# Kernel optimization log

Measured on AMD Instinct MI355X. Metric: run time of the kernel, lower is better.

## Reference

```python
import jax, jax.numpy as jnp
import numpy as np

K = 5  # filter_size
EPS = 1e-5

def conv1x1(x, w):
    # x: [B,Ci,H,W], w: [Co,Ci]
    return jnp.einsum('bihw,oi->bohw', x, w)

def layernorm_c(x, g, b):
    # LayerNorm over channel dim of NCHW (torch permutes to NHWC, norms last dim)
    m = x.mean(axis=1, keepdims=True)
    v = x.var(axis=1, keepdims=True)
    xn = (x - m) / jnp.sqrt(v + EPS)
    return xn * g[None, :, None, None] + b[None, :, None, None]

def conv3x3(x, w):
    return jax.lax.conv_general_dilated(x, w, (1, 1), [(1, 1), (1, 1)],
                                        dimension_numbers=('NCHW', 'OIHW', 'NCHW'))

def apply_dyn_filter(feat, filt):
    # feat: [B,C,H,W]; filt: [B,C*K*K,H,W] ordered as C x (K*K row-major), matching
    # torch .view(B,C,K*K,H,W) and F.unfold channel layout.
    B, C, H, W = feat.shape
    f = filt.reshape(B, C, K * K, H, W)
    p = K // 2
    fp = jnp.pad(feat, ((0, 0), (0, 0), (p, p), (p, p)))  # zero pad, same as F.unfold
    out = jnp.zeros_like(feat)
    for ki in range(K):
        for kj in range(K):
            out = out + fp[:, :, ki:ki + H, kj:kj + W] * f[:, :, ki * K + kj]
    return out


def setup_inputs() -> dict:
    key = jax.random.key(0)
    ks = jax.random.split(key, 9)
    B, Cin, H, W = 1, 64, 128, 128
    Ch = 128
    s = lambda fan: 1.0 / np.sqrt(fan)
    inp = {
        'rgb_high': jax.random.normal(ks[0], (B, Cin, H, W), jnp.float32),
        'event':    jax.random.normal(ks[1], (B, Cin, H, W), jnp.float32),
        'conv_w':   jax.random.normal(ks[2], (Ch, Cin), jnp.float32) * s(Cin),
        'ln_g':     jnp.ones((Ch,), jnp.float32),
        'ln_b':     jnp.zeros((Ch,), jnp.float32),
        'df1_w':    jax.random.normal(ks[3], (Ch, Ch, 3, 3), jnp.float32) * s(Ch * 9),
        'df2_w':    jax.random.normal(ks[4], (Ch * K * K, Ch), jnp.float32) * s(Ch),
        'sp_w':     jax.random.normal(ks[5], (Ch, Ch), jnp.float32) * s(Ch),
        'out_w':    jax.random.normal(ks[6], (Cin, Ch), jnp.float32) * s(Ch),
    }
    return inp


def reference(rgb_high, event, conv_w, ln_g, ln_b, df1_w, df2_w, sp_w, out_w):
    rgb_feat = layernorm_c(conv1x1(rgb_high, conv_w), ln_g, ln_b)
    ev_feat = layernorm_c(conv1x1(event, conv_w), ln_g, ln_b)
    # dynamic filter generator: conv3x3 -> ReLU -> conv1x1 (shared weights)
    rgb_filter = conv1x1(jax.nn.relu(conv3x3(rgb_feat, df1_w)), df2_w)
    ev_filter = conv1x1(jax.nn.relu(conv3x3(ev_feat, df1_w)), df2_w)
    rgb_en = apply_dyn_filter(rgb_feat, rgb_filter)
    ev_en = apply_dyn_filter(ev_feat, ev_filter)
    rgb_filtered = rgb_en * jax.nn.sigmoid(conv1x1(ev_en, sp_w))
    rgb_fused = rgb_en + rgb_filtered + rgb_feat
    rgb_norm = layernorm_c(rgb_fused, ln_g, ln_b)
    return conv1x1(rgb_norm, out_w)
```

## Files before the change

kernel.cpp:

```cpp
#include <hip/hip_runtime.h>
#include <math.h>

#define HW 16384
#define WD 128
#define HD 128
#define CIN 64
#define CH 128
#define EPSV 1e-5f

typedef __attribute__((ext_vector_type(8))) short short8;
typedef __attribute__((ext_vector_type(4))) short short4v;
typedef __attribute__((ext_vector_type(4))) float f32x4;

__device__ __forceinline__ short f2bf(float x) {
  unsigned u = __float_as_uint(x);
  u += 0x7FFFu + ((u >> 16) & 1u);
  return (short)(u >> 16);
}
__device__ __forceinline__ float bf2f(short x) {
  return __uint_as_float(((unsigned)(unsigned short)x) << 16);
}

__global__ __launch_bounds__(256) void k_prep_misc(
    const float* __restrict__ cw, const float* __restrict__ w3,
    const float* __restrict__ spw, const float* __restrict__ outw,
    const float* __restrict__ rgb, const float* __restrict__ ev,
    short* __restrict__ cwp, short* __restrict__ w3p,
    short* __restrict__ spwp, short* __restrict__ outwp,
    short* __restrict__ xT_rgb, short* __restrict__ xT_ev) {
  int idx = blockIdx.x * 256 + threadIdx.x;
  if (idx < 8192) {
    int j = idx & 7, grp = (idx >> 3) & 3, m = (idx >> 5) & 127, q = idx >> 12;
    cwp[idx] = f2bf(cw[m * CIN + q * 32 + grp * 8 + j]);
  } else if (idx < 155648) {
    int i = idx - 8192;
    int j = i & 7, grp = (i >> 3) & 3, m = (i >> 5) & 127, ks = i >> 12;
    int tap = ks >> 2, q = ks & 3;
    int c = q * 32 + grp * 8 + j;
    w3p[i] = f2bf(w3[(m * CH + c) * 9 + tap]);
  } else if (idx < 172032) {
    int i = idx - 155648;
    int j = i & 7, grp = (i >> 3) & 3, m = (i >> 5) & 127, q = i >> 12;
    spwp[i] = f2bf(spw[m * CH + q * 32 + grp * 8 + j]);
  } else if (idx < 180224) {
    int i = idx - 172032;
    int j = i & 7, grp = (i >> 3) & 3, m = (i >> 5) & 63, q = i >> 11;
    outwp[i] = f2bf(outw[m * CH + q * 32 + grp * 8 + j]);
  } else {
    int i = idx - 180224;
    int img = i >> 14, p = i & 16383;
    const float* x = img ? ev : rgb;
    short* xT = img ? xT_ev : xT_rgb;
#pragma unroll
    for (int cb = 0; cb < 8; ++cb) {
      short8 v;
#pragma unroll
      for (int j = 0; j < 8; ++j) v[j] = f2bf(x[(cb * 8 + j) * HW + p]);
      *(short8*)(xT + p * CIN + cb * 8) = v;
    }
  }
}

__global__ __launch_bounds__(256) void k_prep_df2(const float* __restrict__ df2,
                                                  short* __restrict__ df2p) {
  int idx = blockIdx.x * 256 + threadIdx.x;
  int j = idx & 7;
  int slotp = (idx >> 3) & 511;
  int c = idx >> 12;
  int ms = slotp >> 4, k8l = slotp & 15;
  int k8 = k8l ^ (ms & 7);
  int k = k8 * 8 + j;
  int t;
  if (ms < 16) {
    t = (ms >> 2) * 5 + (ms & 3);
  } else {
    int g = (ms >> 2) & 3, r = ms & 3;
    if (g == 0) t = 20 + r;
    else if (g == 1) t = r * 5 + 4;
    else if (g == 2 && r == 0) t = 24;
    else t = -1;
  }
  float v = (t >= 0) ? df2[(c * 25 + t) * CH + k] : 0.f;
  df2p[idx] = f2bf(v);
}

__global__ __launch_bounds__(256) void k_feat_mfma(
    const short* __restrict__ xT_rgb, const short* __restrict__ xT_ev,
    const short* __restrict__ cwp, const float* __restrict__ g,
    const float* __restrict__ b,
    short* __restrict__ featT_rgb, short* __restrict__ featT_ev) {
  __shared__ float sg[CH], sb[CH];
  int tid = threadIdx.x;
  if (tid < CH) { sg[tid] = g[tid]; sb[tid] = b[tid]; }
  __syncthreads();
  const short* xT = blockIdx.z ? xT_ev : xT_rgb;
  short* featT = blockIdx.z ? featT_ev : featT_rgb;
  int wave = tid >> 6, lane = tid & 63, col = lane & 15, grp = lane >> 4;
  int p = blockIdx.x * 64 + wave * 16 + col;

  const short8* bp = (const short8*)(xT + p * CIN);
  short8 bq0 = bp[grp], bq1 = bp[4 + grp];
  const short8* ap = (const short8*)cwp;

  f32x4 acc[8];
#pragma unroll
  for (int mt = 0; mt < 8; ++mt) {
    acc[mt] = (f32x4){0.f, 0.f, 0.f, 0.f};
    short8 a0 = ap[(0 * 128 + mt * 16 + col) * 4 + grp];
    short8 a1 = ap[(1 * 128 + mt * 16 + col) * 4 + grp];
    acc[mt] = __builtin_amdgcn_mfma_f32_16x16x32_bf16(a0, bq0, acc[mt], 0, 0, 0);
    acc[mt] = __builtin_amdgcn_mfma_f32_16x16x32_bf16(a1, bq1, acc[mt], 0, 0, 0);
  }
  float s = 0.f, s2 = 0.f;
#pragma unroll
  for (int mt = 0; mt < 8; ++mt)
#pragma unroll
    for (int r = 0; r < 4; ++r) { float v = acc[mt][r]; s += v; s2 += v * v; }
  s += __shfl_xor(s, 16);  s += __shfl_xor(s, 32);
  s2 += __shfl_xor(s2, 16); s2 += __shfl_xor(s2, 32);
  float mean = s * (1.f / CH);
  float var = s2 * (1.f / CH) - mean * mean;
  float rinv = rsqrtf(var + EPSV);
#pragma unroll
  for (int mt = 0; mt < 8; ++mt) {
    short4v fv;
#pragma unroll
    for (int r = 0; r < 4; ++r) {
      int m = mt * 16 + grp * 4 + r;
      fv[r] = f2bf((acc[mt][r] - mean) * rinv * sg[m] + sb[m]);
    }
    *(short4v*)(featT + p * CH + mt * 16 + grp * 4) = fv;
  }
}

__global__ __launch_bounds__(256) void k_conv3_v4(
    const short* __restrict__ featT_rgb, const short* __restrict__ featT_ev,
    const short* __restrict__ w3p,
    short* __restrict__ rT_rgb, short* __restrict__ rT_ev) {
  __shared__ short sF[108 * 128];
  const short* featT = blockIdx.z ? featT_ev : featT_rgb;
  short* rT = blockIdx.z ? rT_ev : rT_rgb;
  int tid = threadIdx.x, wave = tid >> 6, lane = tid & 63;
  int col = lane & 15, grp = lane >> 4;
  int ty0 = (blockIdx.x >> 3) * 4;
  int tx0 = (blockIdx.x & 7) * 16;

  short8* sF8w = (short8*)sF;
  for (int i = tid; i < 1728; i += 256) {
    int ksl = i & 15, px = i >> 4;
    int yl = px / 18, xl = px % 18;
    int y = ty0 - 1 + yl, x = tx0 - 1 + xl;
    short8 v = {0, 0, 0, 0, 0, 0, 0, 0};
    if ((unsigned)y < (unsigned)HD && (unsigned)x < (unsigned)WD)
      v = *(const short8*)(featT + (y * WD + x) * CH + ksl * 8);
    sF8w[px * 16 + (ksl ^ (xl & 7))] = v;
  }
  __syncthreads();

  int mh = wave & 1;
  int wty = (wave >> 1) * 2;
  f32x4 acc[2][4];
#pragma unroll
  for (int s = 0; s < 2; ++s)
#pragma unroll
    for (int mt = 0; mt < 4; ++mt) acc[s][mt] = (f32x4){0.f, 0.f, 0.f, 0.f};

  const short8* ap = (const short8*)w3p;
  const short8* sF8 = (const short8*)sF;
#pragma unroll
  for (int ks = 0; ks < 36; ++ks) {
    const int tap = ks >> 2, q = ks & 3;
    const int dy = tap / 3 - 1, dx = tap % 3 - 1;
    int xl = col + dx + 1;
    int sl = (q * 4 + grp) ^ (xl & 7);
    int yl0 = wty + dy + 1;
    short8 b0 = sF8[(yl0 * 18 + xl) * 16 + sl];
    short8 b1 = sF8[((yl0 + 1) * 18 + xl) * 16 + sl];
#pragma unroll
    for (int mt = 0; mt < 4; ++mt) {
      short8 a = ap[(ks * 128 + (mh * 4 + mt) * 16 + col) * 4 + grp];
      acc[0][mt] = __builtin_amdgcn_mfma_f32_16x16x32_bf16(a, b0, acc[0][mt], 0, 0, 0);
      acc[1][mt] = __builtin_amdgcn_mfma_f32_16x16x32_bf16(a, b1, acc[1][mt], 0, 0, 0);
    }
  }
#pragma unroll
  for (int s = 0; s < 2; ++s) {
    int p = (ty0 + wty + s) * WD + tx0 + col;
#pragma unroll
    for (int mt = 0; mt < 4; ++mt) {
      short4v v;
#pragma unroll
      for (int r = 0; r < 4; ++r) v[r] = f2bf(fmaxf(acc[s][mt][r], 0.f));
      *(short4v*)(rT + p * CH + (mh * 4 + mt) * 16 + grp * 4) = v;
    }
  }
}

__global__ __launch_bounds__(256, 3) void k_filt_v8(
    const short* __restrict__ featT_rgb, const short* __restrict__ featT_ev,
    const short* __restrict__ rT_rgb, const short* __restrict__ rT_ev,
    const short* __restrict__ df2p,
    short* __restrict__ enT_rgb, short* __restrict__ enT_ev) {
  __shared__ short lsA[4 * 512 * 8];
  __shared__ float fwall[2 * 4 * 408];
  const short* featT = blockIdx.z ? featT_ev : featT_rgb;
  const short* rT = blockIdx.z ? rT_ev : rT_rgb;
  short* enT = blockIdx.z ? enT_ev : enT_rgb;
  int tid = threadIdx.x;
  int wave = tid >> 6, lane = tid & 63;
  int col = lane & 15, grp = lane >> 4;
  int ty0 = (blockIdx.x >> 3) * 16, tx0 = (blockIdx.x & 7) * 16;
  int c0 = blockIdx.y * 4;
  int py0 = ty0 + wave * 4;
  int pxx = tx0 + col;

  {
    const short8* gsrc = (const short8*)(df2p + (size_t)c0 * 4096);
    short8* lA = (short8*)lsA;
    for (int i = tid; i < 2048; i += 256) lA[i] = gsrc[i];
  }
  for (int px = tid; px < 400; px += 256) {
    int wr = px / 20, wc = px % 20;
    int y = ty0 + wr - 2, x = tx0 + wc - 2;
    short4v v = {0, 0, 0, 0};
    if ((unsigned)y < (unsigned)HD && (unsigned)x < (unsigned)WD)
      v = *(const short4v*)(featT + (y * WD + x) * CH + c0);
#pragma unroll
    for (int ci = 0; ci < 4; ++ci) {
      float f = bf2f(v[ci]);
      fwall[ci * 408 + wr * 20 + wc] = f;
      fwall[1632 + ci * 408 + wc * 20 + wr] = f;
    }
  }
  if (tid < 64) {
    int copy = tid >> 5, cc = (tid >> 3) & 3, k = tid & 7;
    fwall[copy * 1632 + cc * 408 + 400 + k] = 0.f;
  }

  short8 rv[4][4];
#pragma unroll
  for (int s = 0; s < 4; ++s) {
    const short8* bp = (const short8*)(rT + ((py0 + s) * WD + pxx) * CH);
#pragma unroll
    for (int q = 0; q < 4; ++q) rv[s][q] = bp[q * 4 + grp];
  }
#pragma unroll
  for (int s = 0; s < 4; ++s)
#pragma unroll
    for (int q = 0; q < 4; ++q) asm volatile("" :: "v"(rv[s][q]));

  int rowb = wave * 4;
  int base0 = (rowb + grp) * 20 + col;
  int step1 = (grp == 1) ? 1 : 20;
  int base1;
  if (grp == 0)      base1 = (rowb + 4) * 20 + col;
  else if (grp == 1) base1 = 1632 + (col + 4) * 20 + rowb;
  else if (grp == 2) base1 = (rowb + 4) * 20 + col + 4;
  else               base1 = rowb * 20 + col;
  __syncthreads();

  const short8* lA8 = (const short8*)lsA;
  short* stp = enT + ((py0 + grp) * WD + pxx) * CH + c0;
  short4v sv;

#pragma unroll
  for (int c = 0; c < 4; ++c) {
    int base0c = c * 512 + col * 16;
    int base1c = base0c + 256;
    short8 a[4];
    f32x4 acc0[4], acc1[4];
#pragma unroll
    for (int q = 0; q < 4; ++q) a[q] = lA8[base0c + (((q << 2) | grp) ^ (col & 7))];
#pragma unroll
    for (int s = 0; s < 4; ++s) {
      acc0[s] = (f32x4){0.f, 0.f, 0.f, 0.f};
#pragma unroll
      for (int q = 0; q < 4; ++q)
        acc0[s] = __builtin_amdgcn_mfma_f32_16x16x32_bf16(a[q], rv[s][q], acc0[s], 0, 0, 0);
    }
#pragma unroll
    for (int q = 0; q < 4; ++q) a[q] = lA8[base1c + (((q << 2) | grp) ^ (col & 7))];
#pragma unroll
    for (int s = 0; s < 4; ++s) {
      acc1[s] = (f32x4){0.f, 0.f, 0.f, 0.f};
#pragma unroll
      for (int q = 0; q < 4; ++q)
        acc1[s] = __builtin_amdgcn_mfma_f32_16x16x32_bf16(a[q], rv[s][q], acc1[s], 0, 0, 0);
    }
    int cb = c * 408;
    float part[4];
#pragma unroll
    for (int s = 0; s < 4; ++s) {
      int i0 = cb + base0 + s * 20;
      int i1 = cb + base1 + s * step1;
      float p = fwall[i0] * acc0[s][0] + fwall[i0 + 1] * acc0[s][1]
              + fwall[i0 + 2] * acc0[s][2] + fwall[i0 + 3] * acc0[s][3]
              + fwall[i1] * acc1[s][0] + fwall[i1 + 1] * acc1[s][1]
              + fwall[i1 + 2] * acc1[s][2] + fwall[i1 + 3] * acc1[s][3];
      part[s] = p;
    }
#pragma unroll
    for (int s = 0; s < 4; ++s) part[s] += __shfl_xor(part[s], 16);
#pragma unroll
    for (int s = 0; s < 4; ++s) part[s] += __shfl_xor(part[s], 32);
    float val = (grp == 0) ? part[0] : (grp == 1) ? part[1]
              : (grp == 2) ? part[2] : part[3];
    sv[c] = f2bf(val);
  }
  *(short4v*)stp = sv;
}

__global__ __launch_bounds__(256) void k_post(
    const short* __restrict__ enT_rgb, const short* __restrict__ enT_ev,
    const short* __restrict__ featT_rgb,
    const short* __restrict__ spwp, const short* __restrict__ outwp,
    const float* __restrict__ g, const float* __restrict__ b,
    float* __restrict__ out) {
  __shared__ short nlds[4][16 * 136];
  __shared__ float sg[CH], sb[CH];
  int tid = threadIdx.x;
  if (tid < CH) { sg[tid] = g[tid]; sb[tid] = b[tid]; }
  __syncthreads();
  int wave = tid >> 6, lane = tid & 63, col = lane & 15, grp = lane >> 4;
  int p = blockIdx.x * 64 + wave * 16 + col;

  const short8* bp = (const short8*)(enT_ev + p * CH);
  short8 bq[4];
#pragma unroll
  for (int q = 0; q < 4; ++q) bq[q] = bp[q * 4 + grp];
  const short8* ap = (const short8*)spwp;
  f32x4 z[8];
#pragma unroll
  for (int mt = 0; mt < 8; ++mt) {
    z[mt] = (f32x4){0.f, 0.f, 0.f, 0.f};
#pragma unroll
    for (int q = 0; q < 4; ++q)
      z[mt] = __builtin_amdgcn_mfma_f32_16x16x32_bf16(
          ap[(q * 128 + mt * 16 + col) * 4 + grp], bq[q], z[mt], 0, 0, 0);
  }

  const short4v* er = (const short4v*)(enT_rgb + p * CH);
  const short4v* fr = (const short4v*)(featT_rgb + p * CH);
  float fused[8][4];
  float s = 0.f, s2 = 0.f;
#pragma unroll
  for (int mt = 0; mt < 8; ++mt) {
    short4v e4 = er[mt * 4 + grp];
    short4v f4 = fr[mt * 4 + grp];
#pragma unroll
    for (int r = 0; r < 4; ++r) {
      float sig = 1.f / (1.f + __expf(-z[mt][r]));
      float f = bf2f(e4[r]) * (1.f + sig) + bf2f(f4[r]);
      fused[mt][r] = f; s += f; s2 += f * f;
    }
  }
  s += __shfl_xor(s, 16);  s += __shfl_xor(s, 32);
  s2 += __shfl_xor(s2, 16); s2 += __shfl_xor(s2, 32);
  float mean = s * (1.f / CH);
  float var = s2 * (1.f / CH) - mean * mean;
  float rinv = rsqrtf(var + EPSV);

  short* nl = &nlds[wave][0];
#pragma unroll
  for (int mt = 0; mt < 8; ++mt) {
    short4v nv;
#pragma unroll
    for (int r = 0; r < 4; ++r) {
      int o = mt * 16 + grp * 4 + r;
      nv[r] = f2bf((fused[mt][r] - mean) * rinv * sg[o] + sb[o]);
    }
    *(short4v*)(nl + col * 136 + mt * 16 + grp * 4) = nv;
  }

  short8 nb[4];
#pragma unroll
  for (int q = 0; q < 4; ++q)
    nb[q] = *(const short8*)(nl + col * 136 + q * 32 + grp * 8);
  const short8* op = (const short8*)outwp;
#pragma unroll
  for (int mt = 0; mt < 4; ++mt) {
    f32x4 oacc = {0.f, 0.f, 0.f, 0.f};
#pragma unroll
    for (int q = 0; q < 4; ++q)
      oacc = __builtin_amdgcn_mfma_f32_16x16x32_bf16(
          op[(q * 64 + mt * 16 + col) * 4 + grp], nb[q], oacc, 0, 0, 0);
#pragma unroll
    for (int r = 0; r < 4; ++r)
      out[(mt * 16 + grp * 4 + r) * HW + p] = oacc[r];
  }
}

extern "C" void kernel_launch(void* const* d_in, const int* in_sizes, int n_in,
                              void* d_out, int out_size, void* d_ws, size_t ws_size,
                              hipStream_t stream) {
  const float* rgb  = (const float*)d_in[0];
  const float* ev   = (const float*)d_in[1];
  const float* cw   = (const float*)d_in[2];
  const float* g    = (const float*)d_in[3];
  const float* b    = (const float*)d_in[4];
  const float* w3   = (const float*)d_in[5];
  const float* df2  = (const float*)d_in[6];
  const float* spw  = (const float*)d_in[7];
  const float* outw = (const float*)d_in[8];
  float* out = (float*)d_out;
  char* wsb = (char*)d_ws;

  const size_t MB = 1u << 20;
  short* featT_rgb = (short*)(wsb);
  short* featT_ev  = (short*)(wsb + 4 * MB);
  short* rT_rgb    = (short*)(wsb + 8 * MB);
  short* rT_ev     = (short*)(wsb + 12 * MB);
  short* enT_rgb   = (short*)(wsb + 16 * MB);
  short* enT_ev    = (short*)(wsb + 20 * MB);
  short* xT_rgb    = (short*)(wsb + 24 * MB);
  short* xT_ev     = (short*)(wsb + 26 * MB);
  short* df2p      = (short*)(wsb + 28 * MB);
  short* w3p       = (short*)(wsb + 29 * MB);
  short* cwp       = (short*)(wsb + 30 * MB);
  short* spwp      = (short*)(wsb + 31 * MB);
  short* outwp     = (short*)(wsb + 32 * MB);

  hipLaunchKernelGGL(k_prep_misc, dim3(832), dim3(256), 0, stream,
                     cw, w3, spw, outw, rgb, ev,
                     cwp, w3p, spwp, outwp, xT_rgb, xT_ev);
  hipLaunchKernelGGL(k_prep_df2, dim3(2048), dim3(256), 0, stream, df2, df2p);
  hipLaunchKernelGGL(k_feat_mfma, dim3(256, 1, 2), dim3(256), 0, stream,
                     xT_rgb, xT_ev, cwp, g, b, featT_rgb, featT_ev);
  hipLaunchKernelGGL(k_conv3_v4, dim3(256, 1, 2), dim3(256), 0, stream,
                     featT_rgb, featT_ev, w3p, rT_rgb, rT_ev);
  hipLaunchKernelGGL(k_filt_v8, dim3(64, 32, 2), dim3(256), 0, stream,
                     featT_rgb, featT_ev, rT_rgb, rT_ev, df2p, enT_rgb, enT_ev);
  hipLaunchKernelGGL(k_post, dim3(256), dim3(256), 0, stream,
                     enT_rgb, enT_ev, featT_rgb, spwp, outwp, g, b, out);
}
```

Before: 135.3 us.

## Merge prep kernels, drop conv3 LDS staging, split post across wave pairs

Merges the df2 weight-packing kernel into the other prep kernel, which saves one launch. The 3x3 conv now reads feature vectors straight from global memory instead of staging a haloed tile in LDS first, removing the LDS fill and barrier at the cost of redundant global and cache reads. The filter kernel's launch bound drops from 3 to 2 blocks per CU, giving it more registers per thread. The post kernel now spreads each 16-pixel group over two waves, each handling half the channels, and combines the LayerNorm statistics through shared memory; this doubles the grid to raise occupancy but adds block barriers.

```diff
diff --git a/kernel.cpp b/kernel.cpp
--- a/kernel.cpp
+++ b/kernel.cpp
@@ -21,13 +21,15 @@
   return __uint_as_float(((unsigned)(unsigned short)x) << 16);
 }
 
-__global__ __launch_bounds__(256) void k_prep_misc(
+__global__ __launch_bounds__(256) void k_prep_all(
     const float* __restrict__ cw, const float* __restrict__ w3,
     const float* __restrict__ spw, const float* __restrict__ outw,
     const float* __restrict__ rgb, const float* __restrict__ ev,
+    const float* __restrict__ df2,
     short* __restrict__ cwp, short* __restrict__ w3p,
     short* __restrict__ spwp, short* __restrict__ outwp,
-    short* __restrict__ xT_rgb, short* __restrict__ xT_ev) {
+    short* __restrict__ xT_rgb, short* __restrict__ xT_ev,
+    short* __restrict__ df2p) {
   int idx = blockIdx.x * 256 + threadIdx.x;
   if (idx < 8192) {
     int j = idx & 7, grp = (idx >> 3) & 3, m = (idx >> 5) & 127, q = idx >> 12;
@@ -46,7 +48,7 @@
     int i = idx - 172032;
     int j = i & 7, grp = (i >> 3) & 3, m = (i >> 5) & 63, q = i >> 11;
     outwp[i] = f2bf(outw[m * CH + q * 32 + grp * 8 + j]);
-  } else {
+  } else if (idx < 212992) {
     int i = idx - 180224;
     int img = i >> 14, p = i & 16383;
     const float* x = img ? ev : rgb;
@@ -58,30 +60,27 @@
       for (int j = 0; j < 8; ++j) v[j] = f2bf(x[(cb * 8 + j) * HW + p]);
       *(short8*)(xT + p * CIN + cb * 8) = v;
     }
-  }
-}
-
-__global__ __launch_bounds__(256) void k_prep_df2(const float* __restrict__ df2,
-                                                  short* __restrict__ df2p) {
-  int idx = blockIdx.x * 256 + threadIdx.x;
-  int j = idx & 7;
-  int slotp = (idx >> 3) & 511;
-  int c = idx >> 12;
-  int ms = slotp >> 4, k8l = slotp & 15;
-  int k8 = k8l ^ (ms & 7);
-  int k = k8 * 8 + j;
-  int t;
-  if (ms < 16) {
-    t = (ms >> 2) * 5 + (ms & 3);
   } else {
-    int g = (ms >> 2) & 3, r = ms & 3;
-    if (g == 0) t = 20 + r;
-    else if (g == 1) t = r * 5 + 4;
-    else if (g == 2 && r == 0) t = 24;
-    else t = -1;
-  }
-  float v = (t >= 0) ? df2[(c * 25 + t) * CH + k] : 0.f;
-  df2p[idx] = f2bf(v);
+    int i = idx - 212992;
+    int j = i & 7;
+    int slotp = (i >> 3) & 511;
+    int c = i >> 12;
+    int ms = slotp >> 4, k8l = slotp & 15;
+    int k8 = k8l ^ (ms & 7);
+    int k = k8 * 8 + j;
+    int t;
+    if (ms < 16) {
+      t = (ms >> 2) * 5 + (ms & 3);
+    } else {
+      int g = (ms >> 2) & 3, r = ms & 3;
+      if (g == 0) t = 20 + r;
+      else if (g == 1) t = r * 5 + 4;
+      else if (g == 2 && r == 0) t = 24;
+      else t = -1;
+    }
+    float v = (t >= 0) ? df2[(c * 25 + t) * CH + k] : 0.f;
+    df2p[i] = f2bf(v);
+  }
 }
 
 __global__ __launch_bounds__(256) void k_feat_mfma(
@@ -133,32 +132,19 @@
   }
 }
 
-__global__ __launch_bounds__(256) void k_conv3_v4(
+__global__ __launch_bounds__(256) void k_conv3_v3(
     const short* __restrict__ featT_rgb, const short* __restrict__ featT_ev,
     const short* __restrict__ w3p,
     short* __restrict__ rT_rgb, short* __restrict__ rT_ev) {
-  __shared__ short sF[108 * 128];
   const short* featT = blockIdx.z ? featT_ev : featT_rgb;
   short* rT = blockIdx.z ? rT_ev : rT_rgb;
   int tid = threadIdx.x, wave = tid >> 6, lane = tid & 63;
   int col = lane & 15, grp = lane >> 4;
-  int ty0 = (blockIdx.x >> 3) * 4;
-  int tx0 = (blockIdx.x & 7) * 16;
-
-  short8* sF8w = (short8*)sF;
-  for (int i = tid; i < 1728; i += 256) {
-    int ksl = i & 15, px = i >> 4;
-    int yl = px / 18, xl = px % 18;
-    int y = ty0 - 1 + yl, x = tx0 - 1 + xl;
-    short8 v = {0, 0, 0, 0, 0, 0, 0, 0};
-    if ((unsigned)y < (unsigned)HD && (unsigned)x < (unsigned)WD)
-      v = *(const short8*)(featT + (y * WD + x) * CH + ksl * 8);
-    sF8w[px * 16 + (ksl ^ (xl & 7))] = v;
-  }
-  __syncthreads();
-
   int mh = wave & 1;
-  int wty = (wave >> 1) * 2;
+  int ty = (blockIdx.x >> 3) * 4 + (wave >> 1) * 2;
+  int tx = (blockIdx.x & 7) * 16;
+  int x = tx + col;
+
   f32x4 acc[2][4];
 #pragma unroll
   for (int s = 0; s < 2; ++s)
@@ -166,16 +152,18 @@
     for (int mt = 0; mt < 4; ++mt) acc[s][mt] = (f32x4){0.f, 0.f, 0.f, 0.f};
 
   const short8* ap = (const short8*)w3p;
-  const short8* sF8 = (const short8*)sF;
 #pragma unroll
   for (int ks = 0; ks < 36; ++ks) {
     const int tap = ks >> 2, q = ks & 3;
     const int dy = tap / 3 - 1, dx = tap % 3 - 1;
-    int xl = col + dx + 1;
-    int sl = (q * 4 + grp) ^ (xl & 7);
-    int yl0 = wty + dy + 1;
-    short8 b0 = sF8[(yl0 * 18 + xl) * 16 + sl];
-    short8 b1 = sF8[((yl0 + 1) * 18 + xl) * 16 + sl];
+    int xs = x + dx;
+    bool xok = (unsigned)xs < (unsigned)WD;
+    int y0 = ty + dy, y1 = ty + 1 + dy;
+    short8 b0 = {0, 0, 0, 0, 0, 0, 0, 0}, b1 = {0, 0, 0, 0, 0, 0, 0, 0};
+    if (xok && (unsigned)y0 < (unsigned)HD)
+      b0 = *(const short8*)(featT + (y0 * WD + xs) * CH + q * 32 + grp * 8);
+    if (xok && (unsigned)y1 < (unsigned)HD)
+      b1 = *(const short8*)(featT + (y1 * WD + xs) * CH + q * 32 + grp * 8);
 #pragma unroll
     for (int mt = 0; mt < 4; ++mt) {
       short8 a = ap[(ks * 128 + (mh * 4 + mt) * 16 + col) * 4 + grp];
@@ -185,7 +173,7 @@
   }
 #pragma unroll
   for (int s = 0; s < 2; ++s) {
-    int p = (ty0 + wty + s) * WD + tx0 + col;
+    int p = (ty + s) * WD + x;
 #pragma unroll
     for (int mt = 0; mt < 4; ++mt) {
       short4v v;
@@ -196,7 +184,7 @@
   }
 }
 
-__global__ __launch_bounds__(256, 3) void k_filt_v8(
+__global__ __launch_bounds__(256, 2) void k_filt_v10(
     const short* __restrict__ featT_rgb, const short* __restrict__ featT_ev,
     const short* __restrict__ rT_rgb, const short* __restrict__ rT_ev,
     const short* __restrict__ df2p,
@@ -310,43 +298,47 @@
   *(short4v*)stp = sv;
 }
 
-__global__ __launch_bounds__(256) void k_post(
+__global__ __launch_bounds__(256) void k_post_v2(
     const short* __restrict__ enT_rgb, const short* __restrict__ enT_ev,
     const short* __restrict__ featT_rgb,
     const short* __restrict__ spwp, const short* __restrict__ outwp,
     const float* __restrict__ g, const float* __restrict__ b,
     float* __restrict__ out) {
-  __shared__ short nlds[4][16 * 136];
+  __shared__ short nlds[2][16 * 136];
+  __shared__ float sst[2][2][16][2];
   __shared__ float sg[CH], sb[CH];
   int tid = threadIdx.x;
   if (tid < CH) { sg[tid] = g[tid]; sb[tid] = b[tid]; }
   __syncthreads();
   int wave = tid >> 6, lane = tid & 63, col = lane & 15, grp = lane >> 4;
-  int p = blockIdx.x * 64 + wave * 16 + col;
+  int pr = wave >> 1, h = wave & 1;
+  int p = blockIdx.x * 32 + pr * 16 + col;
 
   const short8* bp = (const short8*)(enT_ev + p * CH);
   short8 bq[4];
 #pragma unroll
   for (int q = 0; q < 4; ++q) bq[q] = bp[q * 4 + grp];
   const short8* ap = (const short8*)spwp;
-  f32x4 z[8];
-#pragma unroll
-  for (int mt = 0; mt < 8; ++mt) {
+  f32x4 z[4];
+#pragma unroll
+  for (int mt = 0; mt < 4; ++mt) {
+    int mtp = h * 4 + mt;
     z[mt] = (f32x4){0.f, 0.f, 0.f, 0.f};
 #pragma unroll
     for (int q = 0; q < 4; ++q)
       z[mt] = __builtin_amdgcn_mfma_f32_16x16x32_bf16(
-          ap[(q * 128 + mt * 16 + col) * 4 + grp], bq[q], z[mt], 0, 0, 0);
+          ap[(q * 128 + mtp * 16 + col) * 4 + grp], bq[q], z[mt], 0, 0, 0);
   }
 
   const short4v* er = (const short4v*)(enT_rgb + p * CH);
   const short4v* fr = (const short4v*)(featT_rgb + p * CH);
-  float fused[8][4];
+  float fused[4][4];
   float s = 0.f, s2 = 0.f;
 #pragma unroll
-  for (int mt = 0; mt < 8; ++mt) {
-    short4v e4 = er[mt * 4 + grp];
-    short4v f4 = fr[mt * 4 + grp];
+  for (int mt = 0; mt < 4; ++mt) {
+    int mtp = h * 4 + mt;
+    short4v e4 = er[mtp * 4 + grp];
+    short4v f4 = fr[mtp * 4 + grp];
 #pragma unroll
     for (int r = 0; r < 4; ++r) {
       float sig = 1.f / (1.f + __expf(-z[mt][r]));
@@ -356,21 +348,27 @@
   }
   s += __shfl_xor(s, 16);  s += __shfl_xor(s, 32);
   s2 += __shfl_xor(s2, 16); s2 += __shfl_xor(s2, 32);
-  float mean = s * (1.f / CH);
-  float var = s2 * (1.f / CH) - mean * mean;
+  if (grp == 0) { sst[pr][h][col][0] = s; sst[pr][h][col][1] = s2; }
+  __syncthreads();
+  float st  = sst[pr][0][col][0] + sst[pr][1][col][0];
+  float st2 = sst[pr][0][col][1] + sst[pr][1][col][1];
+  float mean = st * (1.f / CH);
+  float var = st2 * (1.f / CH) - mean * mean;
   float rinv = rsqrtf(var + EPSV);
 
-  short* nl = &nlds[wave][0];
-#pragma unroll
-  for (int mt = 0; mt < 8; ++mt) {
+  short* nl = &nlds[pr][0];
+#pragma unroll
+  for (int mt = 0; mt < 4; ++mt) {
+    int mtp = h * 4 + mt;
     short4v nv;
 #pragma unroll
     for (int r = 0; r < 4; ++r) {
-      int o = mt * 16 + grp * 4 + r;
+      int o = mtp * 16 + grp * 4 + r;
       nv[r] = f2bf((fused[mt][r] - mean) * rinv * sg[o] + sb[o]);
     }
-    *(short4v*)(nl + col * 136 + mt * 16 + grp * 4) = nv;
-  }
+    *(short4v*)(nl + col * 136 + mtp * 16 + grp * 4) = nv;
+  }
+  __syncthreads();
 
   short8 nb[4];
 #pragma unroll
@@ -378,15 +376,16 @@
     nb[q] = *(const short8*)(nl + col * 136 + q * 32 + grp * 8);
   const short8* op = (const short8*)outwp;
 #pragma unroll
-  for (int mt = 0; mt < 4; ++mt) {
+  for (int mt2 = 0; mt2 < 2; ++mt2) {
+    int mo = h * 2 + mt2;
     f32x4 oacc = {0.f, 0.f, 0.f, 0.f};
 #pragma unroll
     for (int q = 0; q < 4; ++q)
       oacc = __builtin_amdgcn_mfma_f32_16x16x32_bf16(
-          op[(q * 64 + mt * 16 + col) * 4 + grp], nb[q], oacc, 0, 0, 0);
+          op[(q * 64 + mo * 16 + col) * 4 + grp], nb[q], oacc, 0, 0, 0);
 #pragma unroll
     for (int r = 0; r < 4; ++r)
-      out[(mt * 16 + grp * 4 + r) * HW + p] = oacc[r];
+      out[(mo * 16 + grp * 4 + r) * HW + p] = oacc[r];
   }
 }
 
@@ -420,16 +419,15 @@
   short* spwp      = (short*)(wsb + 31 * MB);
   short* outwp     = (short*)(wsb + 32 * MB);
 
-  hipLaunchKernelGGL(k_prep_misc, dim3(832), dim3(256), 0, stream,
-                     cw, w3, spw, outw, rgb, ev,
-                     cwp, w3p, spwp, outwp, xT_rgb, xT_ev);
-  hipLaunchKernelGGL(k_prep_df2, dim3(2048), dim3(256), 0, stream, df2, df2p);
+  hipLaunchKernelGGL(k_prep_all, dim3(2880), dim3(256), 0, stream,
+                     cw, w3, spw, outw, rgb, ev, df2,
+                     cwp, w3p, spwp, outwp, xT_rgb, xT_ev, df2p);
   hipLaunchKernelGGL(k_feat_mfma, dim3(256, 1, 2), dim3(256), 0, stream,
                      xT_rgb, xT_ev, cwp, g, b, featT_rgb, featT_ev);
-  hipLaunchKernelGGL(k_conv3_v4, dim3(256, 1, 2), dim3(256), 0, stream,
+  hipLaunchKernelGGL(k_conv3_v3, dim3(256, 1, 2), dim3(256), 0, stream,
                      featT_rgb, featT_ev, w3p, rT_rgb, rT_ev);
-  hipLaunchKernelGGL(k_filt_v8, dim3(64, 32, 2), dim3(256), 0, stream,
+  hipLaunchKernelGGL(k_filt_v10, dim3(64, 32, 2), dim3(256), 0, stream,
                      featT_rgb, featT_ev, rT_rgb, rT_ev, df2p, enT_rgb, enT_ev);
-  hipLaunchKernelGGL(k_post, dim3(256), dim3(256), 0, stream,
+  hipLaunchKernelGGL(k_post_v2, dim3(512), dim3(256), 0, stream,
                      enT_rgb, enT_ev, featT_rgb, spwp, outwp, g, b, out);
 }
```

New measurement: 125.6 us. 7.2% less time.
